# Kernel tuning notes

Hardware: AMD Instinct MI355X
Metric: run time of the kernel (lower is better)

## Reference

```python
import jax, jax.numpy as jnp
import numpy as np

B, H, W, C, NH = 4, 64, 64, 512, 16
HD = C // NH
BIAS_LEVEL = 0.1
LN_EPS = 1e-5


def layernorm(x, g, b):
    m = jnp.mean(x, axis=-1, keepdims=True)
    v = jnp.mean(jnp.square(x - m), axis=-1, keepdims=True)
    return (x - m) * jax.lax.rsqrt(v + LN_EPS) * g + b


def partition(x, idx):
    # x: [B, L, C] -> windows [nW, S, C]
    xg = x.reshape(B, H, W, C)
    if idx == 0:  # horizontal strips: window = one row of length W
        return xg.reshape(B * H, W, C)
    else:  # vertical strips: window = one column of length H, ordered by column
        return xg.transpose(0, 2, 1, 3).reshape(B * W, H, C)


def unpartition(w, idx):
    # w: [nW, S, C] -> [B, L, C]
    if idx == 0:
        return w.reshape(B, H * W, C)
    else:
        return w.reshape(B, W, H, C).transpose(0, 2, 1, 3).reshape(B, H * W, C)


def eg_attention(q, k, v, res_x, rpe, idx):
    # q,k,v: [B, L, C]; res_x: [B, L, C]; rpe: [1, NH, S, S]
    S = rpe.shape[-1]
    nW = (B * H * W) // S

    def to_heads(t):
        return partition(t, idx).reshape(nW, S, NH, HD).transpose(0, 2, 1, 3)

    qh, kh, vh = to_heads(q), to_heads(k), to_heads(v)  # [nW, NH, S, HD]
    attn = jnp.einsum('whsd,whtd->whst', qh, kh) + BIAS_LEVEL * rpe
    # gating mask from raw scores
    M = jnp.mean(jnp.abs(attn), axis=(1, 2, 3), keepdims=True)  # [nW,1,1,1]
    M = M / jnp.max(M)
    M = jnp.maximum(M, 0.5)
    # L2-normalize rows, trig transform
    norm = jnp.sqrt(jnp.sum(jnp.square(attn), axis=-1, keepdims=True))
    attn = attn / jnp.maximum(norm, 1e-12)
    attn = 1.0 - jnp.cos(attn * (jnp.pi / 2))
    attn = attn * M
    out = jnp.einsum('whst,whtd->whsd', attn, vh)  # [nW, NH, S, HD]
    out = out.transpose(0, 2, 1, 3).reshape(nW, S, C)
    out = unpartition(out, idx)  # [B, L, C]
    # masked residual: res_x is chunked sequentially (row-major), as in the source
    res = res_x.reshape(nW, S, C) * (1.0 - M[:, 0])
    res = res.reshape(B, H * W, C)
    return out + res


def eg_block(x, rpe, idx, ln1_g, ln1_b, wqkv, wproj, bproj, ln2_g, ln2_b,
             wfc1, bfc1, wfc2, bfc2):
    img = layernorm(x, ln1_g, ln1_b)
    qkv = img @ wqkv  # [B, L, 3C]
    q, k, v = jnp.split(qkv, 3, axis=-1)
    att = eg_attention(q, k, v, x, rpe, idx)
    att = att @ wproj + bproj
    x = x + att
    h = layernorm(x, ln2_g, ln2_b)
    h = jax.nn.gelu(h @ wfc1 + bfc1, approximate=False) @ wfc2 + bfc2
    return x + h


def setup_inputs() -> dict:
    key = jax.random.key(0)
    ks = jax.random.split(key, 16)
    d = {
        'x': jax.random.normal(ks[0], (B, H * W, C), jnp.float32),
        'rpe0': jax.random.normal(ks[1], (1, NH, W, W), jnp.float32),
        'rpe1': jax.random.normal(ks[2], (1, NH, H, H), jnp.float32),
    }
    for i, blk in enumerate(['0', '1']):
        kk = jax.random.split(ks[3 + i], 8)
        d['ln1_g' + blk] = jnp.ones((C,), jnp.float32)
        d['ln1_b' + blk] = jnp.zeros((C,), jnp.float32)
        d['wqkv' + blk] = jax.random.normal(kk[0], (C, 3 * C), jnp.float32) * 0.02
        d['wproj' + blk] = jax.random.normal(kk[1], (C, C), jnp.float32) * 0.02
        d['bproj' + blk] = jnp.zeros((C,), jnp.float32)
        d['ln2_g' + blk] = jnp.ones((C,), jnp.float32)
        d['ln2_b' + blk] = jnp.zeros((C,), jnp.float32)
        d['wfc1_' + blk] = jax.random.normal(kk[2], (C, 4 * C), jnp.float32) * 0.02
        d['bfc1_' + blk] = jnp.zeros((4 * C,), jnp.float32)
        d['wfc2_' + blk] = jax.random.normal(kk[3], (4 * C, C), jnp.float32) * 0.02
        d['bfc2_' + blk] = jnp.zeros((C,), jnp.float32)
    return d


def reference(x, rpe0, rpe1,
              ln1_g0, ln1_b0, wqkv0, wproj0, bproj0, ln2_g0, ln2_b0,
              wfc1_0, bfc1_0, wfc2_0, bfc2_0,
              ln1_g1, ln1_b1, wqkv1, wproj1, bproj1, ln2_g1, ln2_b1,
              wfc1_1, bfc1_1, wfc2_1, bfc2_1):
    x = eg_block(x, rpe0, 0, ln1_g0, ln1_b0, wqkv0, wproj0, bproj0,
                 ln2_g0, ln2_b0, wfc1_0, bfc1_0, wfc2_0, bfc2_0)
    x = eg_block(x, rpe1, 1, ln1_g1, ln1_b1, wqkv1, wproj1, bproj1,
                 ln2_g1, ln2_b1, wfc1_1, bfc1_1, wfc2_1, bfc2_1)
    return x
```

## Files before the change

### kernel.cpp

```cpp
#include <hip/hip_runtime.h>
#include <cstdint>
#include <cstddef>

typedef __bf16 bf16;
typedef __attribute__((ext_vector_type(4))) float f32x4;
typedef __attribute__((ext_vector_type(8))) __bf16 bf16x8;
typedef __attribute__((ext_vector_type(4))) __bf16 bf16x4;

static __device__ __forceinline__ f32x4 mfma16(bf16x8 a, bf16x8 b, f32x4 c) {
    return __builtin_amdgcn_mfma_f32_16x16x32_bf16(a, b, c, 0, 0, 0);
}

#define GLOAD_LDS16(gsrc, ldst)                                              \
    __builtin_amdgcn_global_load_lds(                                        \
        (const __attribute__((address_space(1))) void*)(gsrc),               \
        (__attribute__((address_space(3))) void*)(ldst), 16, 0, 0)

__global__ __launch_bounds__(256)
void transpose_cast(const float* __restrict__ W, bf16* __restrict__ Wt, int K, int N) {
    __shared__ float tile[32][33];
    const int n0 = blockIdx.x * 32, k0 = blockIdx.y * 32;
    const int tx = threadIdx.x & 31, ty = threadIdx.x >> 5;
    #pragma unroll
    for (int i = ty; i < 32; i += 8)
        tile[i][tx] = W[(size_t)(k0 + i) * N + n0 + tx];
    __syncthreads();
    #pragma unroll
    for (int i = ty; i < 32; i += 8)
        Wt[(size_t)(n0 + i) * K + k0 + tx] = (bf16)tile[tx][i];
}

__global__ __launch_bounds__(256)
void ln_kernel(const float* __restrict__ x, const float* __restrict__ g,
               const float* __restrict__ b, bf16* __restrict__ out) {
    const int row = blockIdx.x * 4 + (threadIdx.x >> 6);
    const int lane = threadIdx.x & 63;
    const float* p = x + (size_t)row * 512 + lane * 8;
    const float4 a0 = *(const float4*)p;
    const float4 a1 = *(const float4*)(p + 4);
    float vx[8] = {a0.x, a0.y, a0.z, a0.w, a1.x, a1.y, a1.z, a1.w};
    float s = 0.f, ss = 0.f;
    #pragma unroll
    for (int k = 0; k < 8; ++k) { s += vx[k]; ss += vx[k] * vx[k]; }
    #pragma unroll
    for (int m = 1; m < 64; m <<= 1) {
        s  += __shfl_xor(s, m);
        ss += __shfl_xor(ss, m);
    }
    const float mean = s * (1.0f / 512.0f);
    const float var  = ss * (1.0f / 512.0f) - mean * mean;
    const float inv  = rsqrtf(var + 1e-5f);
    const int c0 = lane * 8;
    const float4 g0 = *(const float4*)&g[c0], g1 = *(const float4*)&g[c0 + 4];
    const float4 b0 = *(const float4*)&b[c0], b1 = *(const float4*)&b[c0 + 4];
    const float gv[8] = {g0.x, g0.y, g0.z, g0.w, g1.x, g1.y, g1.z, g1.w};
    const float bv[8] = {b0.x, b0.y, b0.z, b0.w, b1.x, b1.y, b1.z, b1.w};
    bf16x8 o;
    #pragma unroll
    for (int k = 0; k < 8; ++k)
        o[k] = (bf16)((vx[k] - mean) * inv * gv[k] + bv[k]);
    *(bf16x8*)&out[(size_t)row * 512 + c0] = o;
}

template <int EPI, int KT>
__global__ __launch_bounds__(512, 8)
void gemm_bt(const bf16* __restrict__ A, const bf16* __restrict__ Bt,
             int N, int Krt, const float* __restrict__ bias,
             const float* __restrict__ res, float* __restrict__ outf,
             bf16* __restrict__ outh) {
    const int K = (KT > 0) ? KT : Krt;
    __shared__ __align__(16) bf16 smem[16384];
    auto lsA = [&](int buf) { return smem + buf * 4096; };
    auto lsB = [&](int buf) { return smem + 8192 + buf * 4096; };
    const int nx = gridDim.x;
    const int nwg = nx * gridDim.y;
    const int flat = blockIdx.y * nx + blockIdx.x;
    const int cpx = nwg >> 3;
    const int bswz = (flat & 7) * cpx + (flat >> 3);
    const int bn = bswz % nx, bm = bswz / nx;

    const int tid = threadIdx.x, lane = tid & 63, wv = tid >> 6;
    const int wr = wv >> 2, wc = wv & 3;
    const int l15 = lane & 15, lg = lane >> 4;
    const size_t abase = (size_t)bm * 128 * K;
    const size_t bbase = (size_t)bn * 128 * K;
    const int sr = wv * 16 + (lane >> 2);
    const int ks = ((lane & 3) ^ ((sr >> 1) & 3)) * 8;
    const bf16* aSrc = &A[abase + (size_t)sr * K + ks];
    const bf16* bSrc = &Bt[bbase + (size_t)sr * K + ks];

    f32x4 acc[4][2] = {};

    auto stage = [&](int buf, int kt) {
        GLOAD_LDS16(aSrc + kt, lsA(buf) + wv * 512);
        GLOAD_LDS16(bSrc + kt, lsB(buf) + wv * 512);
    };
    auto compute = [&](int buf) {
        bf16x8 af[4], bfr[2];
        #pragma unroll
        for (int i = 0; i < 4; ++i) {
            const int r = wr * 64 + i * 16 + l15;
            af[i] = *(const bf16x8*)
                (lsA(buf) + r * 32 + ((lg ^ ((r >> 1) & 3)) * 8));
        }
        #pragma unroll
        for (int j = 0; j < 2; ++j) {
            const int r = wc * 32 + j * 16 + l15;
            bfr[j] = *(const bf16x8*)
                (lsB(buf) + r * 32 + ((lg ^ ((r >> 1) & 3)) * 8));
        }
        #pragma unroll
        for (int i = 0; i < 4; ++i)
            #pragma unroll
            for (int j = 0; j < 2; ++j)
                acc[i][j] = mfma16(af[i], bfr[j], acc[i][j]);
    };

    if constexpr (KT > 0) {
        constexpr int NK = KT >> 5;
        stage(0, 0);
        __syncthreads();
        #pragma unroll
        for (int t = 0; t < NK - 1; ++t) {
            stage((t + 1) & 1, (t + 1) * 32);
            compute(t & 1);
            __syncthreads();
        }
        compute((NK - 1) & 1);
        __syncthreads();
    } else {
        const int NK = K >> 5;
        stage(0, 0);
        __syncthreads();
        int cur = 0;
        for (int t = 0; t < NK - 1; ++t) {
            stage(cur ^ 1, (t + 1) * 32);
            compute(cur);
            __syncthreads();
            cur ^= 1;
        }
        compute(cur);
        __syncthreads();
    }

    float* lsW = (float*)smem + wv * 1024;
    const int orow = bm * 128 + wr * 64;
    const int ocol = bn * 128 + wc * 32;
    #pragma unroll
    for (int i = 0; i < 4; ++i) {
        #pragma unroll
        for (int r = 0; r < 4; ++r)
            #pragma unroll
            for (int j = 0; j < 2; ++j)
                lsW[(lg * 4 + r) * 36 + j * 16 + l15] = acc[i][j][r];
        __builtin_amdgcn_s_waitcnt(0);
        if constexpr (EPI == 0 || EPI == 2) {
            const int rl = lane >> 2, c8 = (lane & 3) * 8;
            const float4 v0 = *(const float4*)&lsW[rl * 36 + c8];
            const float4 v1 = *(const float4*)&lsW[rl * 36 + c8 + 4];
            float vv[8] = {v0.x, v0.y, v0.z, v0.w, v1.x, v1.y, v1.z, v1.w};
            if constexpr (EPI == 2) {
                const float4 bb0 = *(const float4*)&bias[ocol + c8];
                const float4 bb1 = *(const float4*)&bias[ocol + c8 + 4];
                const float bv[8] = {bb0.x, bb0.y, bb0.z, bb0.w,
                                     bb1.x, bb1.y, bb1.z, bb1.w};
                #pragma unroll
                for (int e = 0; e < 8; ++e) {
                    const float t = vv[e] + bv[e];
                    vv[e] = 0.5f * t * (1.0f + erff(t * 0.70710678118f));
                }
            }
            bf16x8 o;
            #pragma unroll
            for (int e = 0; e < 8; ++e) o[e] = (bf16)vv[e];
            *(bf16x8*)&outh[(size_t)(orow + i * 16 + rl) * N + ocol + c8] = o;
        } else {
            const int c4 = (lane & 7) * 4;
            const float4 bb = *(const float4*)&bias[ocol + c4];
            #pragma unroll
            for (int ii = 0; ii < 2; ++ii) {
                const int rl = ii * 8 + (lane >> 3);
                const size_t gro = (size_t)(orow + i * 16 + rl) * N + ocol + c4;
                float4 v = *(const float4*)&lsW[rl * 36 + c4];
                const float4 rr = *(const float4*)&res[gro];
                v.x += bb.x + rr.x; v.y += bb.y + rr.y;
                v.z += bb.z + rr.z; v.w += bb.w + rr.w;
                *(float4*)&outf[gro] = v;
            }
        }
    }
}

__global__ __launch_bounds__(256)
void attn_stats(const bf16* __restrict__ qkv, const float* __restrict__ rpe,
                float* __restrict__ Mraw4, int idx) {
    __shared__ float lsum[4];
    const int bid = blockIdx.x;
    const int w = bid >> 2;
    const int tid = threadIdx.x, lane = tid & 63, wv = tid >> 6;
    const int h = (bid & 3) * 4 + wv;
    const int l15 = lane & 15, lg = lane >> 4;
    const long gbase = (idx == 0) ? (long)w * 64 : ((long)(w >> 6) * 4096 + (w & 63));
    const long gstride = (idx == 0) ? 1 : 64;
    bf16x8 kf[4];
    #pragma unroll
    for (int i = 0; i < 4; ++i) {
        const long gs = gbase + (long)(i * 16 + l15) * gstride;
        kf[i] = *(const bf16x8*)&qkv[gs * 1536 + 512 + h * 32 + lg * 8];
    }
    const float* rh = rpe + h * 4096;
    float asum = 0.f;
    #pragma unroll
    for (int mi = 0; mi < 4; ++mi) {
        const long gs = gbase + (long)(mi * 16 + l15) * gstride;
        const bf16x8 qf = *(const bf16x8*)&qkv[gs * 1536 + h * 32 + lg * 8];
        f32x4 sc[4] = {};
        #pragma unroll
        for (int ni = 0; ni < 4; ++ni) sc[ni] = mfma16(qf, kf[ni], sc[ni]);
        #pragma unroll
        for (int r = 0; r < 4; ++r) {
            const int srow = mi * 16 + lg * 4 + r;
            #pragma unroll
            for (int ni = 0; ni < 4; ++ni)
                asum += fabsf(sc[ni][r] + 0.1f * rh[srow * 64 + ni * 16 + l15]);
        }
    }
    #pragma unroll
    for (int m = 1; m < 64; m <<= 1) asum += __shfl_xor(asum, m);
    if (lane == 0) lsum[wv] = asum;
    __syncthreads();
    if (tid == 0) Mraw4[bid] = lsum[0] + lsum[1] + lsum[2] + lsum[3];
}

__global__ __launch_bounds__(256)
void mcalc(const float* __restrict__ Mraw4, float* __restrict__ Mv) {
    __shared__ float red[4];
    const int t = threadIdx.x, lane = t & 63;
    const float v = (Mraw4[t * 4] + Mraw4[t * 4 + 1] + Mraw4[t * 4 + 2] +
                     Mraw4[t * 4 + 3]) * (1.0f / 65536.0f);
    float m = v;
    #pragma unroll
    for (int msk = 1; msk < 64; msk <<= 1) m = fmaxf(m, __shfl_xor(m, msk));
    if (lane == 0) red[t >> 6] = m;
    __syncthreads();
    const float mm = fmaxf(fmaxf(red[0], red[1]), fmaxf(red[2], red[3]));
    Mv[t] = fmaxf(v / mm, 0.5f);
}

__global__ __launch_bounds__(256)
void attn_apply(const bf16* __restrict__ qkv, const float* __restrict__ rpe,
                const float* __restrict__ Mv, const float* __restrict__ xin,
                bf16* __restrict__ attout, int idx) {
    __shared__ __align__(16) bf16 lsP[4][64 * 64];
    __shared__ __align__(16) bf16 lsVt[4][32 * 64];
    const int bid = blockIdx.x;
    const int w = bid >> 2;
    const int tid = threadIdx.x, lane = tid & 63, wv = tid >> 6;
    const int h = (bid & 3) * 4 + wv;
    const int l15 = lane & 15, lg = lane >> 4;
    const long gbase = (idx == 0) ? (long)w * 64 : ((long)(w >> 6) * 4096 + (w & 63));
    const long gstride = (idx == 0) ? 1 : 64;
    const float Mw = Mv[w];
    bf16* P  = lsP[wv];
    bf16* Vt = lsVt[wv];

    {
        const int d4 = (lane & 7) * 4;
        #pragma unroll
        for (int it = 0; it < 8; ++it) {
            const int t = it * 8 + (lane >> 3);
            const bf16x4 v = *(const bf16x4*)
                &qkv[(gbase + (long)t * gstride) * 1536 + 1024 + h * 32 + d4];
            #pragma unroll
            for (int e = 0; e < 4; ++e) {
                const int d = d4 + e;
                Vt[d * 64 + (t ^ ((d & 7) * 8))] = v[e];
            }
        }
    }
    bf16x8 kf[4];
    #pragma unroll
    for (int i = 0; i < 4; ++i) {
        const long gs = gbase + (long)(i * 16 + l15) * gstride;
        kf[i] = *(const bf16x8*)&qkv[gs * 1536 + 512 + h * 32 + lg * 8];
    }
    const float* rh = rpe + h * 4096;
    #pragma unroll
    for (int mi = 0; mi < 4; ++mi) {
        const long gs = gbase + (long)(mi * 16 + l15) * gstride;
        const bf16x8 qf = *(const bf16x8*)&qkv[gs * 1536 + h * 32 + lg * 8];
        f32x4 sc[4] = {};
        #pragma unroll
        for (int ni = 0; ni < 4; ++ni) sc[ni] = mfma16(qf, kf[ni], sc[ni]);
        #pragma unroll
        for (int r = 0; r < 4; ++r) {
            const int srow = mi * 16 + lg * 4 + r;
            float vv[4], ssq = 0.f;
            #pragma unroll
            for (int ni = 0; ni < 4; ++ni) {
                const float v = sc[ni][r] + 0.1f * rh[srow * 64 + ni * 16 + l15];
                vv[ni] = v;
                ssq += v * v;
            }
            ssq += __shfl_xor(ssq, 1);
            ssq += __shfl_xor(ssq, 2);
            ssq += __shfl_xor(ssq, 4);
            ssq += __shfl_xor(ssq, 8);
            const float is = 1.0f / fmaxf(sqrtf(ssq), 1e-12f);
            #pragma unroll
            for (int ni = 0; ni < 4; ++ni) {
                const float v = (1.0f - __cosf(vv[ni] * is * 1.57079632679f)) * Mw;
                const int col = ni * 16 + l15;
                P[srow * 64 + (col ^ ((srow & 7) * 8))] = (bf16)v;
            }
        }
    }
    f32x4 acc[4][2] = {};
    #pragma unroll
    for (int kk = 0; kk < 2; ++kk) {
        bf16x8 bfr[2];
        #pragma unroll
        for (int dj = 0; dj < 2; ++dj) {
            const int d = dj * 16 + l15;
            bfr[dj] = *(const bf16x8*)&Vt[d * 64 + ((kk * 32 + lg * 8) ^ ((d & 7) * 8))];
        }
        #pragma unroll
        for (int mi = 0; mi < 4; ++mi) {
            const int s = mi * 16 + l15;
            const bf16x8 af = *(const bf16x8*)&P[s * 64 + ((kk * 32 + lg * 8) ^ ((s & 7) * 8))];
            #pragma unroll
            for (int dj = 0; dj < 2; ++dj)
                acc[mi][dj] = mfma16(af, bfr[dj], acc[mi][dj]);
        }
    }
    #pragma unroll
    for (int mi = 0; mi < 4; ++mi) {
        #pragma unroll
        for (int r = 0; r < 4; ++r) {
            const int s = mi * 16 + lg * 4 + r;
            const long gg = gbase + (long)s * gstride;
            const float rm = 1.0f - Mv[(int)(gg >> 6)];
            #pragma unroll
            for (int dj = 0; dj < 2; ++dj) {
                const int d = dj * 16 + l15;
                const size_t oidx = (size_t)gg * 512 + h * 32 + d;
                attout[oidx] = (bf16)(acc[mi][dj][r] + xin[oidx] * rm);
            }
        }
    }
}

extern "C" void kernel_launch(void* const* d_in, const int* in_sizes, int n_in,
                              void* d_out, int out_size, void* d_ws, size_t ws_size,
                              hipStream_t stream) {
    const float* x    = (const float*)d_in[0];
    const float* rpe0 = (const float*)d_in[1];
    const float* rpe1 = (const float*)d_in[2];
    auto W = [&](int i) { return (const float*)d_in[i]; };

    char* ws = (char*)d_ws;
    size_t off = 0;
    auto alloc = [&](size_t bytes) {
        void* p = ws + off;
        off += (bytes + 255) & ~(size_t)255;
        return p;
    };
    bf16 *wqkvT[2], *wprojT[2], *wfc1T[2], *wfc2T[2];
    for (int b = 0; b < 2; ++b) {
        wqkvT[b] = (bf16*)alloc((size_t)1536 * 512 * 2);
        wprojT[b] = (bf16*)alloc((size_t)512 * 512 * 2);
        wfc1T[b] = (bf16*)alloc((size_t)2048 * 512 * 2);
        wfc2T[b] = (bf16*)alloc((size_t)512 * 2048 * 2);
    }
    bf16* IMG = (bf16*)alloc((size_t)16384 * 512 * 2);
    bf16* QKV = (bf16*)alloc((size_t)16384 * 1536 * 2);
    bf16* ATT = (bf16*)alloc((size_t)16384 * 512 * 2);
    bf16* H1  = QKV;
    float* X1    = (float*)alloc((size_t)16384 * 512 * 4);
    float* Mraw4 = (float*)alloc(1024 * 4);
    float* Mv    = (float*)alloc(256 * 4);
    float* XMID  = (float*)d_out;

    auto launchT = [&](const float* Wp, bf16* Wt, int K, int N) {
        transpose_cast<<<dim3(N / 32, K / 32), 256, 0, stream>>>(Wp, Wt, K, N);
    };
    launchT(W(5), wqkvT[0], 512, 1536);
    launchT(W(6), wprojT[0], 512, 512);
    launchT(W(10), wfc1T[0], 512, 2048);
    launchT(W(12), wfc2T[0], 2048, 512);
    launchT(W(16), wqkvT[1], 512, 1536);
    launchT(W(17), wprojT[1], 512, 512);
    launchT(W(21), wfc1T[1], 512, 2048);
    launchT(W(23), wfc2T[1], 2048, 512);

    for (int b = 0; b < 2; ++b) {
        const float* xin = (b == 0) ? x : X1;
        const float* rpe = (b == 0) ? rpe0 : rpe1;
        const int base = (b == 0) ? 3 : 14;
        const float* ln1g = W(base + 0);
        const float* ln1b = W(base + 1);
        const float* bproj = W(base + 4);
        const float* ln2g = W(base + 5);
        const float* ln2b = W(base + 6);
        const float* bfc1 = W(base + 8);
        const float* bfc2 = W(base + 10);

        ln_kernel<<<4096, 256, 0, stream>>>(xin, ln1g, ln1b, IMG);
        gemm_bt<0, 512><<<dim3(12, 128), 512, 0, stream>>>(
            IMG, wqkvT[b], 1536, 512, nullptr, nullptr, nullptr, QKV);
        attn_stats<<<1024, 256, 0, stream>>>(QKV, rpe, Mraw4, b);
        mcalc<<<1, 256, 0, stream>>>(Mraw4, Mv);
        attn_apply<<<1024, 256, 0, stream>>>(QKV, rpe, Mv, xin, ATT, b);
        gemm_bt<1, 512><<<dim3(4, 128), 512, 0, stream>>>(
            ATT, wprojT[b], 512, 512, bproj, xin, XMID, nullptr);
        ln_kernel<<<4096, 256, 0, stream>>>(XMID, ln2g, ln2b, IMG);
        gemm_bt<2, 512><<<dim3(16, 128), 512, 0, stream>>>(
            IMG, wfc1T[b], 2048, 512, bfc1, nullptr, nullptr, H1);
        gemm_bt<1, 0><<<dim3(4, 128), 512, 0, stream>>>(
            H1, wfc2T[b], 512, 2048, bfc2, XMID, (b == 0) ? X1 : XMID, nullptr);
    }
    (void)in_sizes; (void)n_in; (void)out_size; (void)ws_size;
}
```

Before: 451.1 us.

## Use 128x64 tiles for N=512 GEMMs and batch weight transposes into one launch

```diff
diff --git a/kernel.cpp b/kernel.cpp
--- a/kernel.cpp
+++ b/kernel.cpp
@@ -16,10 +16,28 @@
         (const __attribute__((address_space(1))) void*)(gsrc),               \
         (__attribute__((address_space(3))) void*)(ldst), 16, 0, 0)
 
+struct TransArgs {
+    const float* W[8];
+    bf16* Wt[8];
+    int K[8];
+    int N[8];
+    int blk0[9];
+};
+
 __global__ __launch_bounds__(256)
-void transpose_cast(const float* __restrict__ W, bf16* __restrict__ Wt, int K, int N) {
+void transpose_all(TransArgs a) {
     __shared__ float tile[32][33];
-    const int n0 = blockIdx.x * 32, k0 = blockIdx.y * 32;
+    const int b = blockIdx.x;
+    int j = 0;
+    #pragma unroll
+    for (int i = 0; i < 7; ++i)
+        if (b >= a.blk0[i + 1]) j = i + 1;
+    const int rel = b - a.blk0[j];
+    const int K = a.K[j], N = a.N[j];
+    const int nxb = N >> 5;
+    const int n0 = (rel % nxb) * 32, k0 = (rel / nxb) * 32;
+    const float* W = a.W[j];
+    bf16* Wt = a.Wt[j];
     const int tx = threadIdx.x & 31, ty = threadIdx.x >> 5;
     #pragma unroll
     for (int i = ty; i < 32; i += 8)
@@ -62,16 +80,19 @@
     *(bf16x8*)&out[(size_t)row * 512 + c0] = o;
 }
 
-template <int EPI, int KT>
+template <int EPI, int KT, int TN>
 __global__ __launch_bounds__(512, 8)
 void gemm_bt(const bf16* __restrict__ A, const bf16* __restrict__ Bt,
              int N, int Krt, const float* __restrict__ bias,
              const float* __restrict__ res, float* __restrict__ outf,
              bf16* __restrict__ outh) {
+    static_assert(TN == 128 || EPI == 1, "TN=64 only with fp32 epilogue");
+    constexpr int NJ = (TN == 128) ? 2 : 1;
+    constexpr int SMEM_ELEMS = 8192 + 2 * TN * 32;
     const int K = (KT > 0) ? KT : Krt;
-    __shared__ __align__(16) bf16 smem[16384];
+    __shared__ __align__(16) bf16 smem[SMEM_ELEMS];
     auto lsA = [&](int buf) { return smem + buf * 4096; };
-    auto lsB = [&](int buf) { return smem + 8192 + buf * 4096; };
+    auto lsB = [&](int buf) { return smem + 8192 + buf * (TN * 32); };
     const int nx = gridDim.x;
     const int nwg = nx * gridDim.y;
     const int flat = blockIdx.y * nx + blockIdx.x;
@@ -83,20 +104,21 @@
     const int wr = wv >> 2, wc = wv & 3;
     const int l15 = lane & 15, lg = lane >> 4;
     const size_t abase = (size_t)bm * 128 * K;
-    const size_t bbase = (size_t)bn * 128 * K;
+    const size_t bbase = (size_t)bn * TN * K;
     const int sr = wv * 16 + (lane >> 2);
     const int ks = ((lane & 3) ^ ((sr >> 1) & 3)) * 8;
     const bf16* aSrc = &A[abase + (size_t)sr * K + ks];
     const bf16* bSrc = &Bt[bbase + (size_t)sr * K + ks];
-
-    f32x4 acc[4][2] = {};
+    const bool doB = (TN == 128) || (wv < 4);
+
+    f32x4 acc[4][NJ] = {};
 
     auto stage = [&](int buf, int kt) {
         GLOAD_LDS16(aSrc + kt, lsA(buf) + wv * 512);
-        GLOAD_LDS16(bSrc + kt, lsB(buf) + wv * 512);
+        if (doB) GLOAD_LDS16(bSrc + kt, lsB(buf) + wv * 512);
     };
     auto compute = [&](int buf) {
-        bf16x8 af[4], bfr[2];
+        bf16x8 af[4], bfr[NJ];
         #pragma unroll
         for (int i = 0; i < 4; ++i) {
             const int r = wr * 64 + i * 16 + l15;
@@ -104,15 +126,15 @@
                 (lsA(buf) + r * 32 + ((lg ^ ((r >> 1) & 3)) * 8));
         }
         #pragma unroll
-        for (int j = 0; j < 2; ++j) {
-            const int r = wc * 32 + j * 16 + l15;
+        for (int j = 0; j < NJ; ++j) {
+            const int r = wc * (16 * NJ) + j * 16 + l15;
             bfr[j] = *(const bf16x8*)
                 (lsB(buf) + r * 32 + ((lg ^ ((r >> 1) & 3)) * 8));
         }
         #pragma unroll
         for (int i = 0; i < 4; ++i)
             #pragma unroll
-            for (int j = 0; j < 2; ++j)
+            for (int j = 0; j < NJ; ++j)
                 acc[i][j] = mfma16(af[i], bfr[j], acc[i][j]);
     };
 
@@ -143,50 +165,70 @@
         __syncthreads();
     }
 
-    float* lsW = (float*)smem + wv * 1024;
     const int orow = bm * 128 + wr * 64;
-    const int ocol = bn * 128 + wc * 32;
-    #pragma unroll
-    for (int i = 0; i < 4; ++i) {
-        #pragma unroll
-        for (int r = 0; r < 4; ++r)
-            #pragma unroll
-            for (int j = 0; j < 2; ++j)
-                lsW[(lg * 4 + r) * 36 + j * 16 + l15] = acc[i][j][r];
-        __builtin_amdgcn_s_waitcnt(0);
-        if constexpr (EPI == 0 || EPI == 2) {
-            const int rl = lane >> 2, c8 = (lane & 3) * 8;
-            const float4 v0 = *(const float4*)&lsW[rl * 36 + c8];
-            const float4 v1 = *(const float4*)&lsW[rl * 36 + c8 + 4];
-            float vv[8] = {v0.x, v0.y, v0.z, v0.w, v1.x, v1.y, v1.z, v1.w};
-            if constexpr (EPI == 2) {
-                const float4 bb0 = *(const float4*)&bias[ocol + c8];
-                const float4 bb1 = *(const float4*)&bias[ocol + c8 + 4];
-                const float bv[8] = {bb0.x, bb0.y, bb0.z, bb0.w,
-                                     bb1.x, bb1.y, bb1.z, bb1.w};
+    const int ocol = bn * TN + wc * (16 * NJ);
+    if constexpr (NJ == 2) {
+        float* lsW = (float*)smem + wv * 1024;
+        #pragma unroll
+        for (int i = 0; i < 4; ++i) {
+            #pragma unroll
+            for (int r = 0; r < 4; ++r)
                 #pragma unroll
-                for (int e = 0; e < 8; ++e) {
-                    const float t = vv[e] + bv[e];
-                    vv[e] = 0.5f * t * (1.0f + erff(t * 0.70710678118f));
+                for (int j = 0; j < 2; ++j)
+                    lsW[(lg * 4 + r) * 36 + j * 16 + l15] = acc[i][j][r];
+            __builtin_amdgcn_s_waitcnt(0);
+            if constexpr (EPI == 0 || EPI == 2) {
+                const int rl = lane >> 2, c8 = (lane & 3) * 8;
+                const float4 v0 = *(const float4*)&lsW[rl * 36 + c8];
+                const float4 v1 = *(const float4*)&lsW[rl * 36 + c8 + 4];
+                float vv[8] = {v0.x, v0.y, v0.z, v0.w, v1.x, v1.y, v1.z, v1.w};
+                if constexpr (EPI == 2) {
+                    const float4 bb0 = *(const float4*)&bias[ocol + c8];
+                    const float4 bb1 = *(const float4*)&bias[ocol + c8 + 4];
+                    const float bv[8] = {bb0.x, bb0.y, bb0.z, bb0.w,
+                                         bb1.x, bb1.y, bb1.z, bb1.w};
+                    #pragma unroll
+                    for (int e = 0; e < 8; ++e) {
+                        const float t = vv[e] + bv[e];
+                        vv[e] = 0.5f * t * (1.0f + erff(t * 0.70710678118f));
+                    }
+                }
+                bf16x8 o;
+                #pragma unroll
+                for (int e = 0; e < 8; ++e) o[e] = (bf16)vv[e];
+                *(bf16x8*)&outh[(size_t)(orow + i * 16 + rl) * N + ocol + c8] = o;
+            } else {
+                const int c4 = (lane & 7) * 4;
+                const float4 bb = *(const float4*)&bias[ocol + c4];
+                #pragma unroll
+                for (int ii = 0; ii < 2; ++ii) {
+                    const int rl = ii * 8 + (lane >> 3);
+                    const size_t gro = (size_t)(orow + i * 16 + rl) * N + ocol + c4;
+                    float4 v = *(const float4*)&lsW[rl * 36 + c4];
+                    const float4 rr = *(const float4*)&res[gro];
+                    v.x += bb.x + rr.x; v.y += bb.y + rr.y;
+                    v.z += bb.z + rr.z; v.w += bb.w + rr.w;
+                    *(float4*)&outf[gro] = v;
                 }
             }
-            bf16x8 o;
-            #pragma unroll
-            for (int e = 0; e < 8; ++e) o[e] = (bf16)vv[e];
-            *(bf16x8*)&outh[(size_t)(orow + i * 16 + rl) * N + ocol + c8] = o;
-        } else {
-            const int c4 = (lane & 7) * 4;
-            const float4 bb = *(const float4*)&bias[ocol + c4];
-            #pragma unroll
-            for (int ii = 0; ii < 2; ++ii) {
-                const int rl = ii * 8 + (lane >> 3);
-                const size_t gro = (size_t)(orow + i * 16 + rl) * N + ocol + c4;
-                float4 v = *(const float4*)&lsW[rl * 36 + c4];
-                const float4 rr = *(const float4*)&res[gro];
-                v.x += bb.x + rr.x; v.y += bb.y + rr.y;
-                v.z += bb.z + rr.z; v.w += bb.w + rr.w;
-                *(float4*)&outf[gro] = v;
-            }
+        }
+    } else {
+        float* lsW = (float*)smem + wv * 320;
+        const int rl = lane >> 2, c4 = (lane & 3) * 4;
+        const float4 bb = *(const float4*)&bias[ocol + c4];
+        #pragma unroll
+        for (int i = 0; i < 4; ++i) {
+            #pragma unroll
+            for (int r = 0; r < 4; ++r)
+                lsW[(lg * 4 + r) * 20 + l15] = acc[i][0][r];
+            __builtin_amdgcn_s_waitcnt(0);
+            const size_t gro = (size_t)(orow + i * 16 + rl) * N + ocol + c4;
+            float4 v = *(const float4*)&lsW[rl * 20 + c4];
+            const float4 rr = *(const float4*)&res[gro];
+            v.x += bb.x + rr.x; v.y += bb.y + rr.y;
+            v.z += bb.z + rr.z; v.w += bb.w + rr.w;
+            *(float4*)&outf[gro] = v;
+            __builtin_amdgcn_s_waitcnt(0);
         }
     }
 }
@@ -381,17 +423,23 @@
     float* Mv    = (float*)alloc(256 * 4);
     float* XMID  = (float*)d_out;
 
-    auto launchT = [&](const float* Wp, bf16* Wt, int K, int N) {
-        transpose_cast<<<dim3(N / 32, K / 32), 256, 0, stream>>>(Wp, Wt, K, N);
-    };
-    launchT(W(5), wqkvT[0], 512, 1536);
-    launchT(W(6), wprojT[0], 512, 512);
-    launchT(W(10), wfc1T[0], 512, 2048);
-    launchT(W(12), wfc2T[0], 2048, 512);
-    launchT(W(16), wqkvT[1], 512, 1536);
-    launchT(W(17), wprojT[1], 512, 512);
-    launchT(W(21), wfc1T[1], 512, 2048);
-    launchT(W(23), wfc2T[1], 2048, 512);
+    TransArgs ta;
+    const int widx[8] = {5, 6, 10, 12, 16, 17, 21, 23};
+    bf16* wdst[8] = {wqkvT[0], wprojT[0], wfc1T[0], wfc2T[0],
+                     wqkvT[1], wprojT[1], wfc1T[1], wfc2T[1]};
+    const int wk[8] = {512, 512, 512, 2048, 512, 512, 512, 2048};
+    const int wn[8] = {1536, 512, 2048, 512, 1536, 512, 2048, 512};
+    int acc_b = 0;
+    for (int i = 0; i < 8; ++i) {
+        ta.W[i] = W(widx[i]);
+        ta.Wt[i] = wdst[i];
+        ta.K[i] = wk[i];
+        ta.N[i] = wn[i];
+        ta.blk0[i] = acc_b;
+        acc_b += (wn[i] / 32) * (wk[i] / 32);
+    }
+    ta.blk0[8] = acc_b;
+    transpose_all<<<acc_b, 256, 0, stream>>>(ta);
 
     for (int b = 0; b < 2; ++b) {
         const float* xin = (b == 0) ? x : X1;
@@ -406,17 +454,17 @@
         const float* bfc2 = W(base + 10);
 
         ln_kernel<<<4096, 256, 0, stream>>>(xin, ln1g, ln1b, IMG);
-        gemm_bt<0, 512><<<dim3(12, 128), 512, 0, stream>>>(
+        gemm_bt<0, 512, 128><<<dim3(12, 128), 512, 0, stream>>>(
             IMG, wqkvT[b], 1536, 512, nullptr, nullptr, nullptr, QKV);
         attn_stats<<<1024, 256, 0, stream>>>(QKV, rpe, Mraw4, b);
         mcalc<<<1, 256, 0, stream>>>(Mraw4, Mv);
         attn_apply<<<1024, 256, 0, stream>>>(QKV, rpe, Mv, xin, ATT, b);
-        gemm_bt<1, 512><<<dim3(4, 128), 512, 0, stream>>>(
+        gemm_bt<1, 512, 64><<<dim3(8, 128), 512, 0, stream>>>(
             ATT, wprojT[b], 512, 512, bproj, xin, XMID, nullptr);
         ln_kernel<<<4096, 256, 0, stream>>>(XMID, ln2g, ln2b, IMG);
-        gemm_bt<2, 512><<<dim3(16, 128), 512, 0, stream>>>(
+        gemm_bt<2, 512, 128><<<dim3(16, 128), 512, 0, stream>>>(
             IMG, wfc1T[b], 2048, 512, bfc1, nullptr, nullptr, H1);
-        gemm_bt<1, 0><<<dim3(4, 128), 512, 0, stream>>>(
+        gemm_bt<1, 0, 64><<<dim3(8, 128), 512, 0, stream>>>(
             H1, wfc2T[b], 512, 2048, bfc2, XMID, (b == 0) ? X1 : XMID, nullptr);
     }
     (void)in_sizes; (void)n_in; (void)out_size; (void)ws_size;
```

After: 464.1 us. 1.03x slower.
